# Kernel tuning notes

Measured on AMD Instinct MI355X. Metric: run time of the kernel, lower is better.

## Reference

```python
import jax, jax.numpy as jnp
import numpy as np


def setup_inputs() -> dict:
    key = jax.random.key(0)
    ks = jax.random.split(key, 6)
    B, N_IN, N_OUT, C_IN, C_OUT, S, NNZ = 16, 6250, 25000, 64, 64, 9, 75000
    x = jax.random.normal(ks[0], (B, N_IN, C_IN), dtype=jnp.float32)
    trans_values = jax.random.uniform(ks[1], (NNZ,), dtype=jnp.float32)
    trans_row = jax.random.randint(ks[2], (NNZ,), 0, N_OUT, dtype=jnp.int32)
    trans_col = jax.random.randint(ks[3], (NNZ,), 0, N_IN, dtype=jnp.int32)
    spiral_indices = jax.random.randint(ks[4], (N_OUT, S), 0, N_OUT, dtype=jnp.int32)
    # Linear(S*C_IN -> C_OUT), kaiming-ish scale
    W = jax.random.normal(ks[5], (S * C_IN, C_OUT), dtype=jnp.float32) * (1.0 / np.sqrt(S * C_IN))
    b = jnp.zeros((C_OUT,), dtype=jnp.float32)
    return {"x": x, "trans_values": trans_values, "trans_row": trans_row,
            "trans_col": trans_col, "spiral_indices": spiral_indices,
            "W": W, "b": b, "n_out": N_OUT}


def reference(x, trans_values, trans_row, trans_col, spiral_indices, W, b, n_out):
    B, N_in, C = x.shape
    # Pool: gather cols, scale by sparse values, scatter-add to rows
    gathered = x[:, trans_col, :] * trans_values[None, :, None]        # [B, nnz, C]
    pooled = jnp.zeros((B, n_out, C), x.dtype).at[:, trans_row].add(gathered)  # [B, n_out, C]
    # SpiralConv: gather spiral neighborhoods, flatten, linear
    S = spiral_indices.shape[1]
    feat = pooled[:, spiral_indices, :].reshape(B, n_out, S * C)       # [B, n_out, S*C]
    out = feat @ W + b                                                 # [B, n_out, C_out]
    return jax.nn.elu(out)
```

## Files before the change

### kernel.cpp

```cpp
#include <hip/hip_runtime.h>

#define B_     16
#define N_IN_  6250
#define N_OUT_ 25000
#define C_     64
#define S_     9
#define NNZ_   75000
#define MT2_   98

typedef __bf16 bf16x8 __attribute__((ext_vector_type(8)));
typedef float floatx4 __attribute__((ext_vector_type(4)));

__device__ inline void async_copy16(const void* g, void* l) {
    __builtin_amdgcn_global_load_lds(
        (const __attribute__((address_space(1))) void*)g,
        (__attribute__((address_space(3))) void*)l, 16, 0, 0);
}


__global__ void hist_kernel(const int* __restrict__ rows, int* __restrict__ counts, int nnz) {
    int i = blockIdx.x * blockDim.x + threadIdx.x;
    if (i < nnz) atomicAdd(&counts[rows[i]], 1);
}

__global__ void scan1_kernel(const int* __restrict__ counts, int* __restrict__ offsets,
                             int* __restrict__ bsum, int n) {
    __shared__ int wsum[16];
    int t = threadIdx.x;
    int wid = t >> 6, lane = t & 63;
    int i = blockIdx.x * 1024 + t;
    int v = (i < n) ? counts[i] : 0;
    int s = v;
    #pragma unroll
    for (int d = 1; d < 64; d <<= 1) {
        int u = __shfl_up(s, d, 64);
        if (lane >= d) s += u;
    }
    if (lane == 63) wsum[wid] = s;
    __syncthreads();
    if (wid == 0 && lane < 16) {
        int ws = wsum[lane];
        #pragma unroll
        for (int d = 1; d < 16; d <<= 1) {
            int u = __shfl_up(ws, d, 64);
            if (lane >= d) ws += u;
        }
        wsum[lane] = ws;
    }
    __syncthreads();
    int wave_off = (wid == 0) ? 0 : wsum[wid - 1];
    int incl = s + wave_off;
    if (i < n) offsets[i] = incl - v;
    if (t == 1023) bsum[blockIdx.x] = incl;
}

__global__ void scan2_kernel(int* __restrict__ bsum, int* __restrict__ offsets, int nblk, int n) {
    if (threadIdx.x == 0) {
        int t = 0;
        for (int i = 0; i < nblk; ++i) { int v = bsum[i]; bsum[i] = t; t += v; }
        offsets[n] = t;
    }
}

__global__ void scan3_kernel(int* __restrict__ offsets, const int* __restrict__ bsum,
                             int* __restrict__ cursor, int n) {
    int i = blockIdx.x * 1024 + threadIdx.x;
    if (i < n) {
        int o = offsets[i] + bsum[blockIdx.x];
        offsets[i] = o;
        cursor[i] = o;
    }
}

__global__ void fill_kernel(const int* __restrict__ rows, const int* __restrict__ cols,
                            const float* __restrict__ vals, int* __restrict__ cursor,
                            int* __restrict__ ecol, float* __restrict__ eval, int nnz) {
    int i = blockIdx.x * blockDim.x + threadIdx.x;
    if (i < nnz) {
        int p = atomicAdd(&cursor[rows[i]], 1);
        ecol[p] = cols[i];
        eval[p] = vals[i];
    }
}

__global__ __launch_bounds__(256) void pool_kernel(
        const float* __restrict__ x, const int* __restrict__ offsets,
        const int* __restrict__ ecol, const float* __restrict__ eval,
        __bf16* __restrict__ pooled) {
    int t = threadIdx.x;
    int wid = t >> 6, lane = t & 63;
    int row = blockIdx.x * 4 + wid;
    int b = lane >> 2;
    int cq = (lane & 3) << 4;
    int beg = offsets[row], end = offsets[row + 1];

    const float* xb = x + (size_t)b * N_IN_ * C_ + cq;
    floatx4 acc[4] = {};

    int col = 0; float v = 0.f;
    if (beg < end) { col = ecol[beg]; v = eval[beg]; }
    for (int k = beg; k < end; ++k) {
        int col2 = 0; float v2 = 0.f;
        if (k + 1 < end) { col2 = ecol[k + 1]; v2 = eval[k + 1]; }
        const floatx4* xp = reinterpret_cast<const floatx4*>(xb + (size_t)col * C_);
        #pragma unroll
        for (int j = 0; j < 4; ++j) acc[j] += xp[j] * v;
        col = col2; v = v2;
    }

    __bf16* op = pooled + ((size_t)b * N_OUT_ + row) * C_ + cq;
    bf16x8 o0, o1;
    #pragma unroll
    for (int j = 0; j < 4; ++j) {
        o0[j]     = (__bf16)acc[0][j];
        o0[j + 4] = (__bf16)acc[1][j];
        o1[j]     = (__bf16)acc[2][j];
        o1[j + 4] = (__bf16)acc[3][j];
    }
    *reinterpret_cast<bf16x8*>(op)     = o0;
    *reinterpret_cast<bf16x8*>(op + 8) = o1;
}

__global__ void convw_kernel(const float* __restrict__ W, __bf16* __restrict__ WtF) {
    int i = blockIdx.x * blockDim.x + threadIdx.x;
    if (i < 72 * 64 * 8) {
        int kb = i >> 9;
        int n  = (i >> 3) & 63;
        int j  = i & 7;
        WtF[i] = (__bf16)W[(kb * 8 + j) * 64 + n];
    }
}

__global__ __launch_bounds__(256, 2) void gemm_kernel(
        const __bf16* __restrict__ pooled, const int* __restrict__ spiral,
        const __bf16* __restrict__ WtF, const float* __restrict__ bias,
        float* __restrict__ out) {
    __shared__ __bf16 Bs[72 * 64 * 8];

    int bx = blockIdx.x;
    int xcd = bx & 7;
    int rr = bx >> 3;
    int half = (rr >= MT2_) ? 1 : 0;
    int mt = rr - half * MT2_;
    int b = xcd + 8 * half;

    int t = threadIdx.x;
    int wave = t >> 6, lane = t & 63;
    int quad = lane >> 4, l16 = lane & 15;
    int mbase = mt * 256 + wave * 64;

    #pragma unroll
    for (int j = 0; j < 18; ++j) {
        int idx = t + j * 256;
        async_copy16((const char*)WtF + (size_t)idx * 16, (char*)Bs + idx * 16);
    }

    int src[4][S_];
    #pragma unroll
    for (int mi = 0; mi < 4; ++mi) {
        int m = mbase + mi * 16 + l16;
        int mc = (m < N_OUT_) ? m : 0;
        const int* sp = spiral + (size_t)mc * S_;
        int4 a0 = *reinterpret_cast<const int4*>(sp);
        int4 a1 = *reinterpret_cast<const int4*>(sp + 4);
        src[mi][0] = a0.x; src[mi][1] = a0.y; src[mi][2] = a0.z; src[mi][3] = a0.w;
        src[mi][4] = a1.x; src[mi][5] = a1.y; src[mi][6] = a1.z; src[mi][7] = a1.w;
        src[mi][8] = sp[8];
    }
    const __bf16* poolb = pooled + (size_t)b * N_OUT_ * C_;

    __syncthreads();

    floatx4 acc[4][4] = {};
    bf16x8 A0[4][2], A1[4][2], A2[4][2], A3[4][2];

    auto loadA = [&](int s, bf16x8 (*A)[2]) {
        #pragma unroll
        for (int mi = 0; mi < 4; ++mi) {
            const __bf16* p = poolb + (size_t)src[mi][s] * C_ + quad * 8;
            A[mi][0] = *reinterpret_cast<const bf16x8*>(p);
            A[mi][1] = *reinterpret_cast<const bf16x8*>(p + 32);
        }
    };
    auto bufFor = [&](int s) -> bf16x8 (*)[2] {
        switch (s & 3) {
            case 0:  return A0;
            case 1:  return A1;
            case 2:  return A2;
            default: return A3;
        }
    };

    loadA(0, A0);
    loadA(1, A1);
    loadA(2, A2);
    #pragma unroll
    for (int s = 0; s < S_; ++s) {
        if (s + 3 < S_) {
            loadA(s + 3, bufFor(s + 3));
            __builtin_amdgcn_sched_barrier(0);
        }
        bf16x8 (*A)[2] = bufFor(s);
        #pragma unroll
        for (int kc = 0; kc < 2; ++kc) {
            #pragma unroll
            for (int nt = 0; nt < 4; ++nt) {
                int kb = s * 8 + kc * 4 + quad;
                bf16x8 bb = *reinterpret_cast<const bf16x8*>(
                    Bs + (((kb << 6) + (nt << 4) + l16) << 3));
                #pragma unroll
                for (int mi = 0; mi < 4; ++mi)
                    acc[mi][nt] = __builtin_amdgcn_mfma_f32_16x16x32_bf16(
                        A[mi][kc], bb, acc[mi][nt], 0, 0, 0);
            }
        }
    }

    float* outb = out + (size_t)b * N_OUT_ * C_;
    #pragma unroll
    for (int mi = 0; mi < 4; ++mi) {
        #pragma unroll
        for (int nt = 0; nt < 4; ++nt) {
            float bn = bias[nt * 16 + l16];
            #pragma unroll
            for (int i = 0; i < 4; ++i) {
                int mm = mbase + mi * 16 + quad * 4 + i;
                if (mm < N_OUT_) {
                    float v = acc[mi][nt][i] + bn;
                    v = (v > 0.0f) ? v : expm1f(v);
                    __builtin_nontemporal_store(v, &outb[(size_t)mm * C_ + nt * 16 + l16]);
                }
            }
        }
    }
}

extern "C" void kernel_launch(void* const* d_in, const int* in_sizes, int n_in,
                              void* d_out, int out_size, void* d_ws, size_t ws_size,
                              hipStream_t stream) {
    const float* x      = (const float*)d_in[0];
    const float* tvals  = (const float*)d_in[1];
    const int*   trow   = (const int*)d_in[2];
    const int*   tcol   = (const int*)d_in[3];
    const int*   spiral = (const int*)d_in[4];
    const float* W      = (const float*)d_in[5];
    const float* bias   = (const float*)d_in[6];
    float* out = (float*)d_out;

    char* ws = (char*)d_ws;
    size_t off = 0;
    auto alloc = [&](size_t bytes) -> void* {
        void* p = ws + off;
        off += (bytes + 255) & ~(size_t)255;
        return p;
    };
    __bf16* pooled  = (__bf16*)alloc((size_t)B_ * N_OUT_ * C_ * 2);
    __bf16* WtF     = (__bf16*)alloc(72 * 64 * 8 * 2);
    int*    cursor  = (int*)alloc(N_OUT_ * 4);
    int*    offsets = (int*)alloc((N_OUT_ + 1) * 4);
    int*    ecol    = (int*)alloc(NNZ_ * 4);
    float*  eval    = (float*)alloc(NNZ_ * 4);
    int*    counts  = (int*)alloc(N_OUT_ * 4);
    int*    bsum    = (int*)alloc(32 * 4);

    const int NBLK = (N_OUT_ + 1023) / 1024;
    hipMemsetAsync(counts, 0, N_OUT_ * 4, stream);
    hist_kernel<<<(NNZ_ + 255) / 256, 256, 0, stream>>>(trow, counts, NNZ_);
    scan1_kernel<<<NBLK, 1024, 0, stream>>>(counts, offsets, bsum, N_OUT_);
    scan2_kernel<<<1, 64, 0, stream>>>(bsum, offsets, NBLK, N_OUT_);
    scan3_kernel<<<NBLK, 1024, 0, stream>>>(offsets, bsum, cursor, N_OUT_);
    fill_kernel<<<(NNZ_ + 255) / 256, 256, 0, stream>>>(trow, tcol, tvals, cursor, ecol, eval, NNZ_);
    pool_kernel<<<N_OUT_ / 4, 256, 0, stream>>>(x, offsets, ecol, eval, pooled);
    convw_kernel<<<(72 * 64 * 8 + 255) / 256, 256, 0, stream>>>(W, WtF);
    gemm_kernel<<<8 * (2 * MT2_), 256, 0, stream>>>(pooled, spiral, WtF, bias, out);
}
```

Before: 285.3 us.

## Fuse preprocessing kernels into a single cooperative grid-synced kernel

Merges the counter reset, weight conversion, histogram, scan, CSR fill and pooling steps into one cooperative kernel separated by grid-wide syncs. This replaces several small launches and a memset to cut launch and inter-kernel gaps. In exchange, the prefix scan now runs serially in a single block, and pooling uses a persistent grid-stride loop with a fixed grid. Both may reduce parallelism.

```diff
diff --git a/kernel.cpp b/kernel.cpp
--- a/kernel.cpp
+++ b/kernel.cpp
@@ -1,4 +1,7 @@
 #include <hip/hip_runtime.h>
+#include <hip/hip_cooperative_groups.h>
+
+namespace cg = cooperative_groups;
 
 #define B_     16
 #define N_IN_  6250
@@ -8,6 +11,10 @@
 #define NNZ_   75000
 #define MT2_   98
 
+#define PREP_GRID  512
+#define PREP_BLOCK 512
+#define PREP_THREADS (PREP_GRID * PREP_BLOCK)
+
 typedef __bf16 bf16x8 __attribute__((ext_vector_type(8)));
 typedef float floatx4 __attribute__((ext_vector_type(4)));
 
@@ -17,117 +24,117 @@
         (__attribute__((address_space(3))) void*)l, 16, 0, 0);
 }
 
-
-__global__ void hist_kernel(const int* __restrict__ rows, int* __restrict__ counts, int nnz) {
-    int i = blockIdx.x * blockDim.x + threadIdx.x;
-    if (i < nnz) atomicAdd(&counts[rows[i]], 1);
-}
-
-__global__ void scan1_kernel(const int* __restrict__ counts, int* __restrict__ offsets,
-                             int* __restrict__ bsum, int n) {
-    __shared__ int wsum[16];
+__global__ __launch_bounds__(PREP_BLOCK, 4) void prep_kernel(
+        const float* __restrict__ x, const int* __restrict__ trow,
+        const int* __restrict__ tcol, const float* __restrict__ tvals,
+        const float* __restrict__ W,
+        int* __restrict__ counts, int* __restrict__ offsets,
+        int* __restrict__ cursor, int* __restrict__ ecol,
+        float* __restrict__ eval, __bf16* __restrict__ WtF,
+        __bf16* __restrict__ pooled) {
+    cg::grid_group grid = cg::this_grid();
     int t = threadIdx.x;
-    int wid = t >> 6, lane = t & 63;
-    int i = blockIdx.x * 1024 + t;
-    int v = (i < n) ? counts[i] : 0;
-    int s = v;
-    #pragma unroll
-    for (int d = 1; d < 64; d <<= 1) {
-        int u = __shfl_up(s, d, 64);
-        if (lane >= d) s += u;
-    }
-    if (lane == 63) wsum[wid] = s;
-    __syncthreads();
-    if (wid == 0 && lane < 16) {
-        int ws = wsum[lane];
-        #pragma unroll
-        for (int d = 1; d < 16; d <<= 1) {
-            int u = __shfl_up(ws, d, 64);
-            if (lane >= d) ws += u;
-        }
-        wsum[lane] = ws;
-    }
-    __syncthreads();
-    int wave_off = (wid == 0) ? 0 : wsum[wid - 1];
-    int incl = s + wave_off;
-    if (i < n) offsets[i] = incl - v;
-    if (t == 1023) bsum[blockIdx.x] = incl;
-}
-
-__global__ void scan2_kernel(int* __restrict__ bsum, int* __restrict__ offsets, int nblk, int n) {
-    if (threadIdx.x == 0) {
-        int t = 0;
-        for (int i = 0; i < nblk; ++i) { int v = bsum[i]; bsum[i] = t; t += v; }
-        offsets[n] = t;
-    }
-}
-
-__global__ void scan3_kernel(int* __restrict__ offsets, const int* __restrict__ bsum,
-                             int* __restrict__ cursor, int n) {
-    int i = blockIdx.x * 1024 + threadIdx.x;
-    if (i < n) {
-        int o = offsets[i] + bsum[blockIdx.x];
-        offsets[i] = o;
-        cursor[i] = o;
-    }
-}
-
-__global__ void fill_kernel(const int* __restrict__ rows, const int* __restrict__ cols,
-                            const float* __restrict__ vals, int* __restrict__ cursor,
-                            int* __restrict__ ecol, float* __restrict__ eval, int nnz) {
-    int i = blockIdx.x * blockDim.x + threadIdx.x;
-    if (i < nnz) {
-        int p = atomicAdd(&cursor[rows[i]], 1);
-        ecol[p] = cols[i];
-        eval[p] = vals[i];
-    }
-}
-
-__global__ __launch_bounds__(256) void pool_kernel(
-        const float* __restrict__ x, const int* __restrict__ offsets,
-        const int* __restrict__ ecol, const float* __restrict__ eval,
-        __bf16* __restrict__ pooled) {
-    int t = threadIdx.x;
-    int wid = t >> 6, lane = t & 63;
-    int row = blockIdx.x * 4 + wid;
-    int b = lane >> 2;
-    int cq = (lane & 3) << 4;
-    int beg = offsets[row], end = offsets[row + 1];
-
-    const float* xb = x + (size_t)b * N_IN_ * C_ + cq;
-    floatx4 acc[4] = {};
-
-    int col = 0; float v = 0.f;
-    if (beg < end) { col = ecol[beg]; v = eval[beg]; }
-    for (int k = beg; k < end; ++k) {
-        int col2 = 0; float v2 = 0.f;
-        if (k + 1 < end) { col2 = ecol[k + 1]; v2 = eval[k + 1]; }
-        const floatx4* xp = reinterpret_cast<const floatx4*>(xb + (size_t)col * C_);
-        #pragma unroll
-        for (int j = 0; j < 4; ++j) acc[j] += xp[j] * v;
-        col = col2; v = v2;
-    }
-
-    __bf16* op = pooled + ((size_t)b * N_OUT_ + row) * C_ + cq;
-    bf16x8 o0, o1;
-    #pragma unroll
-    for (int j = 0; j < 4; ++j) {
-        o0[j]     = (__bf16)acc[0][j];
-        o0[j + 4] = (__bf16)acc[1][j];
-        o1[j]     = (__bf16)acc[2][j];
-        o1[j + 4] = (__bf16)acc[3][j];
-    }
-    *reinterpret_cast<bf16x8*>(op)     = o0;
-    *reinterpret_cast<bf16x8*>(op + 8) = o1;
-}
-
-__global__ void convw_kernel(const float* __restrict__ W, __bf16* __restrict__ WtF) {
-    int i = blockIdx.x * blockDim.x + threadIdx.x;
-    if (i < 72 * 64 * 8) {
+    int gid = blockIdx.x * PREP_BLOCK + t;
+
+    for (int i = gid; i < N_OUT_; i += PREP_THREADS) counts[i] = 0;
+    for (int i = gid; i < 72 * 64 * 8; i += PREP_THREADS) {
         int kb = i >> 9;
         int n  = (i >> 3) & 63;
         int j  = i & 7;
         WtF[i] = (__bf16)W[(kb * 8 + j) * 64 + n];
+    }
+    __threadfence();
+    grid.sync();
+
+    for (int i = gid; i < NNZ_; i += PREP_THREADS)
+        atomicAdd(&counts[trow[i]], 1);
+    __threadfence();
+    grid.sync();
+
+    if (blockIdx.x == 0) {
+        __shared__ int wsum[8];
+        __shared__ int carry;
+        int wid = t >> 6, lane = t & 63;
+        if (t == 0) carry = 0;
+        __syncthreads();
+        for (int base = 0; base < N_OUT_; base += PREP_BLOCK) {
+            int i = base + t;
+            int v = (i < N_OUT_) ? counts[i] : 0;
+            int s = v;
+            #pragma unroll
+            for (int d = 1; d < 64; d <<= 1) {
+                int u = __shfl_up(s, d, 64);
+                if (lane >= d) s += u;
+            }
+            if (lane == 63) wsum[wid] = s;
+            __syncthreads();
+            if (wid == 0 && lane < 8) {
+                int ws = wsum[lane];
+                #pragma unroll
+                for (int d = 1; d < 8; d <<= 1) {
+                    int u = __shfl_up(ws, d, 64);
+                    if (lane >= d) ws += u;
+                }
+                wsum[lane] = ws;
+            }
+            __syncthreads();
+            int wave_off = (wid == 0) ? 0 : wsum[wid - 1];
+            int incl = s + wave_off + carry;
+            if (i < N_OUT_) {
+                int o = incl - v;
+                offsets[i] = o;
+                cursor[i] = o;
+            }
+            __syncthreads();
+            if (t == PREP_BLOCK - 1) carry = incl;
+            __syncthreads();
+        }
+        if (t == 0) offsets[N_OUT_] = carry;
+    }
+    __threadfence();
+    grid.sync();
+
+    for (int i = gid; i < NNZ_; i += PREP_THREADS) {
+        int p = atomicAdd(&cursor[trow[i]], 1);
+        ecol[p] = tcol[i];
+        eval[p] = tvals[i];
+    }
+    __threadfence();
+    grid.sync();
+
+    {
+        int wid = t >> 6, lane = t & 63;
+        int gw = blockIdx.x * (PREP_BLOCK / 64) + wid;
+        const int NWAVES = PREP_GRID * (PREP_BLOCK / 64);
+        int b = lane >> 2;
+        int cq = (lane & 3) << 4;
+        const float* xb = x + (size_t)b * N_IN_ * C_ + cq;
+
+        for (int row = gw; row < N_OUT_; row += NWAVES) {
+            int beg = offsets[row], end = offsets[row + 1];
+            floatx4 acc[4] = {};
+            int col = 0; float v = 0.f;
+            if (beg < end) { col = ecol[beg]; v = eval[beg]; }
+            for (int k = beg; k < end; ++k) {
+                int col2 = 0; float v2 = 0.f;
+                if (k + 1 < end) { col2 = ecol[k + 1]; v2 = eval[k + 1]; }
+                const floatx4* xp = reinterpret_cast<const floatx4*>(xb + (size_t)col * C_);
+                #pragma unroll
+                for (int j = 0; j < 4; ++j) acc[j] += xp[j] * v;
+                col = col2; v = v2;
+            }
+            __bf16* op = pooled + ((size_t)b * N_OUT_ + row) * C_ + cq;
+            bf16x8 o0, o1;
+            #pragma unroll
+            for (int j = 0; j < 4; ++j) {
+                o0[j]     = (__bf16)acc[0][j];
+                o0[j + 4] = (__bf16)acc[1][j];
+                o1[j]     = (__bf16)acc[2][j];
+                o1[j + 4] = (__bf16)acc[3][j];
+            }
+            *reinterpret_cast<bf16x8*>(op)     = o0;
+            *reinterpret_cast<bf16x8*>(op + 8) = o1;
+        }
     }
 }
 
@@ -261,16 +268,14 @@
     int*    ecol    = (int*)alloc(NNZ_ * 4);
     float*  eval    = (float*)alloc(NNZ_ * 4);
     int*    counts  = (int*)alloc(N_OUT_ * 4);
-    int*    bsum    = (int*)alloc(32 * 4);
-
-    const int NBLK = (N_OUT_ + 1023) / 1024;
-    hipMemsetAsync(counts, 0, N_OUT_ * 4, stream);
-    hist_kernel<<<(NNZ_ + 255) / 256, 256, 0, stream>>>(trow, counts, NNZ_);
-    scan1_kernel<<<NBLK, 1024, 0, stream>>>(counts, offsets, bsum, N_OUT_);
-    scan2_kernel<<<1, 64, 0, stream>>>(bsum, offsets, NBLK, N_OUT_);
-    scan3_kernel<<<NBLK, 1024, 0, stream>>>(offsets, bsum, cursor, N_OUT_);
-    fill_kernel<<<(NNZ_ + 255) / 256, 256, 0, stream>>>(trow, tcol, tvals, cursor, ecol, eval, NNZ_);
-    pool_kernel<<<N_OUT_ / 4, 256, 0, stream>>>(x, offsets, ecol, eval, pooled);
-    convw_kernel<<<(72 * 64 * 8 + 255) / 256, 256, 0, stream>>>(W, WtF);
+
+    void* prep_args[] = {
+        (void*)&x, (void*)&trow, (void*)&tcol, (void*)&tvals, (void*)&W,
+        (void*)&counts, (void*)&offsets, (void*)&cursor, (void*)&ecol,
+        (void*)&eval, (void*)&WtF, (void*)&pooled
+    };
+    hipLaunchCooperativeKernel((const void*)prep_kernel,
+                               dim3(PREP_GRID), dim3(PREP_BLOCK),
+                               prep_args, 0, stream);
     gemm_kernel<<<8 * (2 * MT2_), 256, 0, stream>>>(pooled, spiral, WtF, bias, out);
 }
```

Result: slower. 747.6 us (+162.1%).

## Remap pool work for per-XCD batch locality and fuse init kernels

Applied to the files above, without the earlier changes.

Pool blocks are remapped so that each XCD handles only two batches, keeping their slice of x resident in that XCD's L2. Each thread now accumulates one float4 per nonzero instead of four. The counts memset and the weight conversion are merged into a single init kernel to cut launch count. A scheduling barrier in the GEMM prefetch loop is also removed. The risk is lower per-thread memory parallelism and four times as many pool blocks.

```diff
diff --git a/kernel.cpp b/kernel.cpp
--- a/kernel.cpp
+++ b/kernel.cpp
@@ -9,12 +9,25 @@
 #define MT2_   98
 
 typedef __bf16 bf16x8 __attribute__((ext_vector_type(8)));
+typedef __bf16 bf16x4 __attribute__((ext_vector_type(4)));
 typedef float floatx4 __attribute__((ext_vector_type(4)));
 
 __device__ inline void async_copy16(const void* g, void* l) {
     __builtin_amdgcn_global_load_lds(
         (const __attribute__((address_space(1))) void*)g,
         (__attribute__((address_space(3))) void*)l, 16, 0, 0);
+}
+
+__global__ void init_kernel(const float* __restrict__ W, __bf16* __restrict__ WtF,
+                            int* __restrict__ counts) {
+    int i = blockIdx.x * blockDim.x + threadIdx.x;
+    if (i < N_OUT_) counts[i] = 0;
+    if (i < 72 * 64 * 8) {
+        int kb = i >> 9;
+        int n  = (i >> 3) & 63;
+        int j  = i & 7;
+        WtF[i] = (__bf16)W[(kb * 8 + j) * 64 + n];
+    }
 }
 
 
@@ -87,48 +100,33 @@
         const float* __restrict__ x, const int* __restrict__ offsets,
         const int* __restrict__ ecol, const float* __restrict__ eval,
         __bf16* __restrict__ pooled) {
+    int bx = blockIdx.x;
+    int xcd = bx & 7;
+    int rg = bx >> 3;
     int t = threadIdx.x;
     int wid = t >> 6, lane = t & 63;
-    int row = blockIdx.x * 4 + wid;
-    int b = lane >> 2;
-    int cq = (lane & 3) << 4;
+    int r2  = lane >> 5;
+    int b   = xcd + 8 * ((lane >> 4) & 1);
+    int l16 = lane & 15;
+    int row = rg * 8 + wid * 2 + r2;
+
+    const float* xb = x + (size_t)b * N_IN_ * C_ + l16 * 4;
     int beg = offsets[row], end = offsets[row + 1];
 
-    const float* xb = x + (size_t)b * N_IN_ * C_ + cq;
-    floatx4 acc[4] = {};
-
+    floatx4 acc = {};
     int col = 0; float v = 0.f;
     if (beg < end) { col = ecol[beg]; v = eval[beg]; }
     for (int k = beg; k < end; ++k) {
         int col2 = 0; float v2 = 0.f;
         if (k + 1 < end) { col2 = ecol[k + 1]; v2 = eval[k + 1]; }
-        const floatx4* xp = reinterpret_cast<const floatx4*>(xb + (size_t)col * C_);
-        #pragma unroll
-        for (int j = 0; j < 4; ++j) acc[j] += xp[j] * v;
+        acc += *reinterpret_cast<const floatx4*>(xb + (size_t)col * C_) * v;
         col = col2; v = v2;
     }
 
-    __bf16* op = pooled + ((size_t)b * N_OUT_ + row) * C_ + cq;
-    bf16x8 o0, o1;
-    #pragma unroll
-    for (int j = 0; j < 4; ++j) {
-        o0[j]     = (__bf16)acc[0][j];
-        o0[j + 4] = (__bf16)acc[1][j];
-        o1[j]     = (__bf16)acc[2][j];
-        o1[j + 4] = (__bf16)acc[3][j];
-    }
-    *reinterpret_cast<bf16x8*>(op)     = o0;
-    *reinterpret_cast<bf16x8*>(op + 8) = o1;
-}
-
-__global__ void convw_kernel(const float* __restrict__ W, __bf16* __restrict__ WtF) {
-    int i = blockIdx.x * blockDim.x + threadIdx.x;
-    if (i < 72 * 64 * 8) {
-        int kb = i >> 9;
-        int n  = (i >> 3) & 63;
-        int j  = i & 7;
-        WtF[i] = (__bf16)W[(kb * 8 + j) * 64 + n];
-    }
+    bf16x4 o;
+    #pragma unroll
+    for (int j = 0; j < 4; ++j) o[j] = (__bf16)acc[j];
+    *reinterpret_cast<bf16x4*>(pooled + ((size_t)b * N_OUT_ + row) * C_ + l16 * 4) = o;
 }
 
 __global__ __launch_bounds__(256, 2) void gemm_kernel(
@@ -198,7 +196,6 @@
     for (int s = 0; s < S_; ++s) {
         if (s + 3 < S_) {
             loadA(s + 3, bufFor(s + 3));
-            __builtin_amdgcn_sched_barrier(0);
         }
         bf16x8 (*A)[2] = bufFor(s);
         #pragma unroll
@@ -264,13 +261,12 @@
     int*    bsum    = (int*)alloc(32 * 4);
 
     const int NBLK = (N_OUT_ + 1023) / 1024;
-    hipMemsetAsync(counts, 0, N_OUT_ * 4, stream);
+    init_kernel<<<(72 * 64 * 8 + 255) / 256, 256, 0, stream>>>(W, WtF, counts);
     hist_kernel<<<(NNZ_ + 255) / 256, 256, 0, stream>>>(trow, counts, NNZ_);
     scan1_kernel<<<NBLK, 1024, 0, stream>>>(counts, offsets, bsum, N_OUT_);
     scan2_kernel<<<1, 64, 0, stream>>>(bsum, offsets, NBLK, N_OUT_);
     scan3_kernel<<<NBLK, 1024, 0, stream>>>(offsets, bsum, cursor, N_OUT_);
     fill_kernel<<<(NNZ_ + 255) / 256, 256, 0, stream>>>(trow, tcol, tvals, cursor, ecol, eval, NNZ_);
-    pool_kernel<<<N_OUT_ / 4, 256, 0, stream>>>(x, offsets, ecol, eval, pooled);
-    convw_kernel<<<(72 * 64 * 8 + 255) / 256, 256, 0, stream>>>(W, WtF);
+    pool_kernel<<<8 * (N_OUT_ / 8), 256, 0, stream>>>(x, offsets, ecol, eval, pooled);
     gemm_kernel<<<8 * (2 * MT2_), 256, 0, stream>>>(pooled, spiral, WtF, bias, out);
 }
```

After: 291.9 us. +2.3%, slower.
